# Kernel optimization log

Hardware: AMD Instinct MI355X
Metric: run time of the kernel (lower is better)

The kernel has to match this reference:

```python
import jax, jax.numpy as jnp
import numpy as np

B, T, C, H = 2, 2048, 1024, 16
HD = C // H  # head_dim = 64
NEG_INF = float('-inf')


def setup_inputs() -> dict:
    key = jax.random.key(0)
    ks = jax.random.split(key, 5)
    x = jax.random.normal(ks[0], (B, T, C), dtype=jnp.float32)
    # causal additive mask [T, T]: 0 on/below diagonal, -inf above
    causal = jnp.where(jnp.tril(jnp.ones((T, T), dtype=bool)), 0.0, NEG_INF).astype(jnp.float32)
    # pad the last 256 key positions of every batch element
    key_padding_mask = (jnp.arange(T)[None, :] >= (T - 256)) & jnp.ones((B, 1), dtype=bool)
    scale = 1.0 / np.sqrt(C)
    W_qkv = jax.random.normal(ks[1], (C, 3 * C), dtype=jnp.float32) * scale
    b_qkv = jnp.zeros((3 * C,), dtype=jnp.float32)
    W_out = jax.random.normal(ks[2], (C, C), dtype=jnp.float32) * scale
    b_out = jnp.zeros((C,), dtype=jnp.float32)
    return {
        'x': x,
        'attn_mask': causal,
        'key_padding_mask': key_padding_mask,
        'W_qkv': W_qkv,
        'b_qkv': b_qkv,
        'W_out': W_out,
        'b_out': b_out,
    }


def reference(x, attn_mask, key_padding_mask, W_qkv, b_qkv, W_out, b_out):
    Bx, Tx, Cx = x.shape
    # fused QKV projection -> [B, T, 3, H, HD]
    qkv = (x @ W_qkv + b_qkv).reshape(Bx, Tx, 3, H, HD)
    q = jnp.transpose(qkv[:, :, 0], (0, 2, 1, 3))  # [B, H, T, HD]
    k = jnp.transpose(qkv[:, :, 1], (0, 2, 1, 3))
    v = jnp.transpose(qkv[:, :, 2], (0, 2, 1, 3))
    # scores [B, H, T, T]
    scores = jnp.einsum('bhqd,bhkd->bhqk', q, k) / np.sqrt(HD)
    scores = scores + attn_mask[None, None, :, :]
    scores = jnp.where(key_padding_mask[:, None, None, :], NEG_INF, scores)
    probs = jax.nn.softmax(scores, axis=-1)
    out = jnp.einsum('bhqk,bhkd->bhqd', probs, v)  # [B, H, T, HD]
    out = jnp.transpose(out, (0, 2, 1, 3)).reshape(Bx, Tx, Cx)
    return out @ W_out + b_out
```

## Files before the change

kernel.cpp:

```cpp
#include <hip/hip_runtime.h>
#include <hip/hip_bf16.h>


typedef __attribute__((ext_vector_type(8))) short short8;
typedef __attribute__((ext_vector_type(4))) float f32x4;
typedef __attribute__((ext_vector_type(16))) float f32x16;
typedef __attribute__((ext_vector_type(4))) unsigned int u32x4;
typedef __attribute__((ext_vector_type(4))) unsigned short ushort4v;

#define MFMA_BF16 __builtin_amdgcn_mfma_f32_16x16x32_bf16
#define MFMA32 __builtin_amdgcn_mfma_f32_32x32x16_bf16
#define EXP2 __builtin_amdgcn_exp2f

__device__ __forceinline__ unsigned short f2bf(float f) {
  unsigned int u = __builtin_bit_cast(unsigned int, f);
  u += 0x7fffu + ((u >> 16) & 1u);
  return (unsigned short)(u >> 16);
}

__device__ __forceinline__ unsigned cvtpk_bf16(float lo, float hi) {
  unsigned r;
  asm("v_cvt_pk_bf16_f32 %0, %1, %2" : "=v"(r) : "v"(lo), "v"(hi));
  return r;
}

__device__ __forceinline__ short8 make_pa(unsigned cA, unsigned cB, unsigned cC, unsigned cD) {
  asm volatile("v_permlane32_swap_b32 %0, %1" : "+v"(cA), "+v"(cC));
  asm volatile("v_permlane32_swap_b32 %0, %1" : "+v"(cB), "+v"(cD));
  u32x4 wv = {cA, cB, cC, cD};
  return __builtin_bit_cast(short8, wv);
}

__device__ __forceinline__ void conv_x_body(const float* __restrict__ x,
                                            unsigned short* __restrict__ xb, int bid) {
  const int i = (bid * 256 + threadIdx.x) * 8;
  const float4 v0 = *reinterpret_cast<const float4*>(x + i);
  const float4 v1 = *reinterpret_cast<const float4*>(x + i + 4);
  short8 o;
  o[0] = (short)f2bf(v0.x); o[1] = (short)f2bf(v0.y);
  o[2] = (short)f2bf(v0.z); o[3] = (short)f2bf(v0.w);
  o[4] = (short)f2bf(v1.x); o[5] = (short)f2bf(v1.y);
  o[6] = (short)f2bf(v1.z); o[7] = (short)f2bf(v1.w);
  *reinterpret_cast<short8*>(xb + i) = o;
}

__device__ __forceinline__ void convT_body256(const float* __restrict__ W,
                                              unsigned short* __restrict__ WT,
                                              int Ncols, int bid, unsigned short* L) {
  const int t = threadIdx.x;
  const int kt = bid & 15, nt = bid >> 4;
  const int k0 = kt << 6, n0 = nt << 6;
#pragma unroll
  for (int it = 0; it < 4; ++it) {
    const int flat = it * 256 + t;
    const int kk = flat >> 4, c4 = (flat & 15) << 2;
    const float4 v = *reinterpret_cast<const float4*>(W + (k0 + kk) * Ncols + n0 + c4);
    L[(c4 + 0) * 72 + kk] = f2bf(v.x);
    L[(c4 + 1) * 72 + kk] = f2bf(v.y);
    L[(c4 + 2) * 72 + kk] = f2bf(v.z);
    L[(c4 + 3) * 72 + kk] = f2bf(v.w);
  }
  __syncthreads();
#pragma unroll
  for (int it = 0; it < 2; ++it) {
    const int flat = it * 256 + t;
    const int nn = flat >> 3, k8 = (flat & 7) << 3;
    *reinterpret_cast<short8*>(WT + (n0 + nn) * 1024 + k0 + k8) =
        *reinterpret_cast<const short8*>(&L[nn * 72 + k8]);
  }
}

__device__ __forceinline__ void convT_body512(const float* __restrict__ W,
                                              unsigned short* __restrict__ WT,
                                              int Ncols, int bid, unsigned short* L) {
  const int t = threadIdx.x;
  const int kt = bid & 15, nt = bid >> 4;
  const int k0 = kt << 6, n0 = nt << 6;
#pragma unroll
  for (int it = 0; it < 2; ++it) {
    const int flat = it * 512 + t;
    const int kk = flat >> 4, c4 = (flat & 15) << 2;
    const float4 v = *reinterpret_cast<const float4*>(W + (k0 + kk) * Ncols + n0 + c4);
    L[(c4 + 0) * 72 + kk] = f2bf(v.x);
    L[(c4 + 1) * 72 + kk] = f2bf(v.y);
    L[(c4 + 2) * 72 + kk] = f2bf(v.z);
    L[(c4 + 3) * 72 + kk] = f2bf(v.w);
  }
  __syncthreads();
  {
    const int nn = t >> 3, k8 = (t & 7) << 3;
    *reinterpret_cast<short8*>(WT + (n0 + nn) * 1024 + k0 + k8) =
        *reinterpret_cast<const short8*>(&L[nn * 72 + k8]);
  }
}

__global__ __launch_bounds__(256) void pre_kernel(const float* __restrict__ x,
                                                  unsigned short* __restrict__ xb,
                                                  const float* __restrict__ Wqkv,
                                                  unsigned short* __restrict__ WQT) {
  __shared__ unsigned short L[64 * 72];
  if (blockIdx.x < 2048) conv_x_body(x, xb, blockIdx.x);
  else convT_body256(Wqkv, WQT, 3072, blockIdx.x - 2048, L);
}

__device__ __forceinline__ void stage_tile512(const unsigned short* __restrict__ g,
                                              int row0, int k0,
                                              unsigned short* lds, int t) {
  const int lane = t & 63, w = t >> 6;
  const int rsub = lane >> 3;
  const int col16 = lane & 7;
#pragma unroll
  for (int i = 0; i < 2; ++i) {
    const int c = w * 2 + i;
    const int row = c * 8 + rsub;
    const unsigned short* gp =
        g + (row0 + row) * 1024 + k0 + ((col16 ^ rsub) << 3);
    unsigned short* lp = lds + c * 512;
    __builtin_amdgcn_global_load_lds(
        (const __attribute__((address_space(1))) unsigned int*)gp,
        (__attribute__((address_space(3))) unsigned int*)lp, 16, 0, 0);
  }
}

__device__ __forceinline__ short8 frag_read(const unsigned short* lds, int row, int colB) {
  return *reinterpret_cast<const short8*>(
      reinterpret_cast<const char*>(lds) + row * 128 + (colB ^ ((row & 7) << 4)));
}

__device__ __forceinline__ void gemm_step8(const unsigned short* Ab, const unsigned short* Bb,
                                           int wr, int wc, int lm, int lg, f32x4 acc[2][4]) {
#pragma unroll
  for (int ks = 0; ks < 2; ++ks) {
    short8 af[2], bfr[4];
#pragma unroll
    for (int i = 0; i < 2; ++i)
      af[i] = frag_read(Ab, wr * 32 + i * 16 + lm, ks * 64 + lg * 16);
#pragma unroll
    for (int j = 0; j < 4; ++j)
      bfr[j] = frag_read(Bb, wc * 64 + j * 16 + lm, ks * 64 + lg * 16);
#pragma unroll
    for (int i = 0; i < 2; ++i)
#pragma unroll
      for (int j = 0; j < 4; ++j)
        acc[i][j] = MFMA_BF16(af[i], bfr[j], acc[i][j], 0, 0, 0);
  }
}

__global__ __launch_bounds__(512, 4) void qkv_gemm_kernel(
    const unsigned short* __restrict__ xb,
    const unsigned short* __restrict__ Bt,
    const float* __restrict__ bias,
    unsigned short* __restrict__ ws) {
  __shared__ unsigned short LDSu[32768];
  const int t = threadIdx.x;
  const int bm = blockIdx.x & 31;
  const int bn = blockIdx.x >> 5;
  const int m0 = bm << 7, n0 = bn << 7;
  const int lane = t & 63, wid = t >> 6;
  const int wr = wid & 3, wc = wid >> 2;
  const int lm = lane & 15, lg = lane >> 4;
  f32x4 acc[2][4] = {};

  stage_tile512(xb, m0, 0, LDSu, t);
  stage_tile512(Bt, n0, 0, LDSu + 16384, t);
  asm volatile("s_waitcnt vmcnt(0)" ::: "memory");
  __syncthreads();
  for (int kt = 0; kt < 16; ++kt) {
    const int cur = kt & 1;
    if (kt < 15) {
      stage_tile512(xb, m0, (kt + 1) * 64, LDSu + (cur ^ 1) * 8192, t);
      stage_tile512(Bt, n0, (kt + 1) * 64, LDSu + 16384 + (cur ^ 1) * 8192, t);
    }
    gemm_step8(LDSu + cur * 8192, LDSu + 16384 + cur * 8192, wr, wc, lm, lg, acc);
    asm volatile("s_waitcnt vmcnt(0)" ::: "memory");
    __syncthreads();
  }

  const int which = n0 >> 10;
  if (which == 2) {
#pragma unroll
    for (int j = 0; j < 4; ++j) {
      const int col = wc * 64 + j * 16 + lm;
      const float bv = bias[n0 + col];
#pragma unroll
      for (int i = 0; i < 2; ++i)
#pragma unroll
        for (int r = 0; r < 4; ++r)
          LDSu[col * 136 + wr * 32 + i * 16 + lg * 4 + r] = f2bf(acc[i][j][r] + bv);
    }
    __syncthreads();
    const int bb = m0 >> 11, tt0 = m0 & 2047;
    unsigned short* dstbase = ws + 8388608 + bb * 2097152;
#pragma unroll
    for (int it = 0; it < 4; ++it) {
      const int flat = it * 512 + t;
      const int c = flat >> 4, r8 = (flat & 15) << 3;
      const short8 v = *reinterpret_cast<const short8*>(&LDSu[c * 136 + r8]);
      const int col0 = n0 + c;
      const int h = (col0 >> 6) & 15, d = col0 & 63;
      *reinterpret_cast<short8*>(dstbase + h * 131072 + d * 2048 + tt0 + r8) = v;
    }
  } else {
    const float scl = (which == 0) ? 0.18033688011112042f : 1.0f;
#pragma unroll
    for (int j = 0; j < 4; ++j) {
      const int col = wc * 64 + j * 16 + lm;
      const float bv = bias[n0 + col];
#pragma unroll
      for (int i = 0; i < 2; ++i)
#pragma unroll
        for (int r = 0; r < 4; ++r)
          LDSu[(wr * 32 + i * 16 + lg * 4 + r) * 136 + col] = f2bf((acc[i][j][r] + bv) * scl);
    }
    __syncthreads();
    unsigned short* dstbase = ws + which * 4194304;
#pragma unroll
    for (int it = 0; it < 4; ++it) {
      const int flat = it * 512 + t;
      const int row = flat >> 4, c = flat & 15;
      const short8 v = *reinterpret_cast<const short8*>(&LDSu[row * 136 + c * 8]);
      const int col0 = n0 + c * 8;
      const int h = (col0 >> 6) & 15, d = col0 & 63;
      const int grow = m0 + row;
      const int bb = grow >> 11, tt = grow & 2047;
      *reinterpret_cast<short8*>(dstbase + bb * 2097152 + h * 131072 + tt * 64 + d) = v;
    }
  }
}

__device__ __forceinline__ void stage_one(const unsigned short* __restrict__ src,
                                          int stride, unsigned short* lds, int t) {
  const int lane = t & 63;
  const int row = t >> 3;
  const int rsub = lane >> 3;
  const int col16 = lane & 7;
  const unsigned short* gp = src + row * stride + ((col16 ^ rsub) << 3);
  unsigned short* lp = lds + (t >> 6) * 512;
  __builtin_amdgcn_global_load_lds(
      (const __attribute__((address_space(1))) unsigned int*)gp,
      (__attribute__((address_space(3))) unsigned int*)lp, 16, 0, 0);
}

__device__ __forceinline__ short8 lds_frag64(const unsigned short* lds, int row, int colB) {
  return *reinterpret_cast<const short8*>(
      reinterpret_cast<const char*>(lds) + row * 128 + (colB ^ ((row & 7) << 4)));
}

__device__ __forceinline__ void attn_body(const unsigned short* __restrict__ qkv,
                                          unsigned short* __restrict__ att,
                                          unsigned short* S,
                                          int bid) {
  const int bh = bid & 31;
  const int grp = bid >> 5;
  const int qblk = (bid < 256) ? (15 - grp) : (grp - 8);
  const int q0blk = qblk << 7;
  const int t = threadIdx.x;
  const int w = t >> 6, w4 = w & 3, od = w >> 2;
  const int lane = t & 63;
  const int l31 = lane & 31, hi = lane >> 5;
  const int qrow_local = ((l31 >> 3) << 5) + (w4 << 3) + (l31 & 7);
  const int q_lane = q0blk + qrow_local;

  const unsigned short* Qp = qkv + bh * 131072;
  const unsigned short* Kp = qkv + 4194304 + bh * 131072;
  const unsigned short* Vtp = qkv + 8388608 + bh * 131072;
  unsigned short* KT = S;
  unsigned short* VT = S + 16384;

  short8 qf[4];
#pragma unroll
  for (int ds = 0; ds < 4; ++ds)
    qf[ds] = *reinterpret_cast<const short8*>(Qp + q_lane * 64 + ds * 16 + hi * 8);

  f32x16 o0, o1;
#pragma unroll
  for (int r = 0; r < 16; ++r) { o0[r] = 0.f; o1[r] = 0.f; }
  float mrun = -1e30f, lrun = 0.f;
  const int nkt_raw = 2 * qblk + 2;
  const int nkt = nkt_raw < 28 ? nkt_raw : 28;
  const int npair = nkt >> 1;
  const int qwmax = q0blk + 96 + (w4 << 3) + 7;
  const int qwmin = q0blk + (w4 << 3);

  stage_one(Kp, 64, KT, t);
  stage_one(Kp + 4096, 64, KT + 4096, t);
  stage_one(Vtp, 2048, VT, t);
  stage_one(Vtp + 64, 2048, VT + 4096, t);
  asm volatile("s_waitcnt vmcnt(0)" ::: "memory");
  __syncthreads();

  for (int i = 0; i < npair; ++i) {
    if (i + 1 < npair) {
      const int nb = (i + 1) & 1;
      stage_one(Kp + (2 * i + 2) * 4096, 64, KT + nb * 8192, t);
      stage_one(Kp + (2 * i + 3) * 4096, 64, KT + nb * 8192 + 4096, t);
      stage_one(Vtp + (2 * i + 2) * 64, 2048, VT + nb * 8192, t);
      stage_one(Vtp + (2 * i + 3) * 64, 2048, VT + nb * 8192 + 4096, t);
    }
    const int kt = 2 * i + od;
    const int k0 = kt << 6;
    if (k0 <= qwmax) {
      const unsigned short* Kl = KT + (i & 1) * 8192 + od * 4096;
      const unsigned short* Vl = VT + (i & 1) * 8192 + od * 4096;
      f32x16 s0, s1;
#pragma unroll
      for (int r = 0; r < 16; ++r) { s0[r] = 0.f; s1[r] = 0.f; }
      __builtin_amdgcn_s_setprio(1);
#pragma unroll
      for (int ds = 0; ds < 4; ++ds) {
        short8 ka = lds_frag64(Kl, l31, ds * 32 + hi * 16);
        short8 kb = lds_frag64(Kl, 32 + l31, ds * 32 + hi * 16);
        s0 = MFMA32(ka, qf[ds], s0, 0, 0, 0);
        s1 = MFMA32(kb, qf[ds], s1, 0, 0, 0);
      }
      __builtin_amdgcn_s_setprio(0);
      if (k0 + 63 > qwmin) {
        const int qrel = q_lane - k0;
        const int kb4 = hi << 2;
#pragma unroll
        for (int r = 0; r < 16; ++r) {
          const int cr = (r & 3) + ((r >> 2) << 3) + kb4;
          s0[r] = (cr > qrel) ? -1e30f : s0[r];
          s1[r] = (cr + 32 > qrel) ? -1e30f : s1[r];
        }
      }
      float mx[8];
#pragma unroll
      for (int r = 0; r < 8; ++r)
        mx[r] = fmaxf(fmaxf(s0[r], s0[r + 8]), fmaxf(s1[r], s1[r + 8]));
#pragma unroll
      for (int r = 0; r < 4; ++r) mx[r] = fmaxf(mx[r], mx[r + 4]);
      float mt = fmaxf(fmaxf(mx[0], mx[1]), fmaxf(mx[2], mx[3]));
      mt = fmaxf(mt, __shfl_xor(mt, 32));
      if (__any(mt > mrun + 8.f)) {
        const float mnew = fmaxf(mrun, mt);
        const float sf = EXP2(mrun - mnew);
        mrun = mnew;
        lrun *= sf;
#pragma unroll
        for (int r = 0; r < 16; ++r) { o0[r] *= sf; o1[r] *= sf; }
      }
#pragma unroll
      for (int r = 0; r < 16; ++r) {
        s0[r] = EXP2(s0[r] - mrun);
        s1[r] = EXP2(s1[r] - mrun);
      }
      float sm[8];
#pragma unroll
      for (int r = 0; r < 8; ++r)
        sm[r] = (s0[r] + s0[r + 8]) + (s1[r] + s1[r + 8]);
#pragma unroll
      for (int r = 0; r < 4; ++r) sm[r] += sm[r + 4];
      float rs = (sm[0] + sm[1]) + (sm[2] + sm[3]);
      rs += __shfl_xor(rs, 32);
      lrun += rs;
      unsigned c0[8], c1[8];
#pragma unroll
      for (int j = 0; j < 8; ++j) {
        c0[j] = cvtpk_bf16(s0[2 * j], s0[2 * j + 1]);
        c1[j] = cvtpk_bf16(s1[2 * j], s1[2 * j + 1]);
      }
      const short8 pa0 = make_pa(c0[0], c0[1], c0[2], c0[3]);
      const short8 pa1 = make_pa(c0[4], c0[5], c0[6], c0[7]);
      const short8 pa2 = make_pa(c1[0], c1[1], c1[2], c1[3]);
      const short8 pa3 = make_pa(c1[4], c1[5], c1[6], c1[7]);
      __builtin_amdgcn_s_setprio(1);
      {
        short8 va = lds_frag64(Vl, l31, 0 + hi * 16);
        short8 vb = lds_frag64(Vl, 32 + l31, 0 + hi * 16);
        o0 = MFMA32(va, pa0, o0, 0, 0, 0);
        o1 = MFMA32(vb, pa0, o1, 0, 0, 0);
      }
      {
        short8 va = lds_frag64(Vl, l31, 32 + hi * 16);
        short8 vb = lds_frag64(Vl, 32 + l31, 32 + hi * 16);
        o0 = MFMA32(va, pa1, o0, 0, 0, 0);
        o1 = MFMA32(vb, pa1, o1, 0, 0, 0);
      }
      {
        short8 va = lds_frag64(Vl, l31, 64 + hi * 16);
        short8 vb = lds_frag64(Vl, 32 + l31, 64 + hi * 16);
        o0 = MFMA32(va, pa2, o0, 0, 0, 0);
        o1 = MFMA32(vb, pa2, o1, 0, 0, 0);
      }
      {
        short8 va = lds_frag64(Vl, l31, 96 + hi * 16);
        short8 vb = lds_frag64(Vl, 32 + l31, 96 + hi * 16);
        o0 = MFMA32(va, pa3, o0, 0, 0, 0);
        o1 = MFMA32(vb, pa3, o1, 0, 0, 0);
      }
      __builtin_amdgcn_s_setprio(0);
    }
    asm volatile("s_waitcnt vmcnt(0)" ::: "memory");
    __syncthreads();
  }

  float* M = reinterpret_cast<float*>(S);
  if (od == 1) {
    float* Mb = M + (w4 * 64 + lane) * 36;
#pragma unroll
    for (int i2 = 0; i2 < 4; ++i2) {
      f32x4 a = {o0[4 * i2], o0[4 * i2 + 1], o0[4 * i2 + 2], o0[4 * i2 + 3]};
      f32x4 b = {o1[4 * i2], o1[4 * i2 + 1], o1[4 * i2 + 2], o1[4 * i2 + 3]};
      *reinterpret_cast<f32x4*>(Mb + 4 * i2) = a;
      *reinterpret_cast<f32x4*>(Mb + 16 + 4 * i2) = b;
    }
    Mb[32] = mrun;
    Mb[33] = lrun;
  }
  __syncthreads();
  if (od == 0) {
    const float* Mb = M + (w4 * 64 + lane) * 36;
    const float m_o = Mb[32], l_o = Mb[33];
    const float mstar = fmaxf(mrun, m_o);
    const float a = EXP2(mrun - mstar);
    const float bsc = EXP2(m_o - mstar);
    const float inv = 1.f / (lrun * a + l_o * bsc);
    const float fa = a * inv, fb = bsc * inv;
    const int bb = bh >> 4, h = bh & 15;
    unsigned short* ob = att + (bb * 2048 + q_lane) * 1024 + h * 64;
#pragma unroll
    for (int i = 0; i < 4; ++i) {
      ushort4v p0, p1;
#pragma unroll
      for (int r = 0; r < 4; ++r) {
        p0[r] = f2bf(o0[4 * i + r] * fa + Mb[4 * i + r] * fb);
        p1[r] = f2bf(o1[4 * i + r] * fa + Mb[16 + 4 * i + r] * fb);
      }
      const int d0 = 8 * i + 4 * hi;
      *reinterpret_cast<ushort4v*>(ob + d0) = p0;
      *reinterpret_cast<ushort4v*>(ob + 32 + d0) = p1;
    }
  }
}

__global__ __launch_bounds__(512, 4) void attn_wout_kernel(
    const unsigned short* __restrict__ qkv,
    unsigned short* __restrict__ att,
    const float* __restrict__ Wout,
    unsigned short* __restrict__ WOT) {
  __shared__ unsigned short S[32768];
  if (blockIdx.x < 512) attn_body(qkv, att, S, blockIdx.x);
  else convT_body512(Wout, WOT, 1024, blockIdx.x - 512, S);
}

__global__ __launch_bounds__(512, 4) void out_gemm_kernel(
    const unsigned short* __restrict__ A,
    const unsigned short* __restrict__ Bt,
    const float* __restrict__ bias,
    float* __restrict__ out) {
  __shared__ unsigned short LDSu[32768];
  const int t = threadIdx.x;
  const int bm = blockIdx.x & 31;
  const int bn = blockIdx.x >> 5;
  const int m0 = bm << 7, n0 = bn << 7;
  const int lane = t & 63, wid = t >> 6;
  const int wr = wid & 3, wc = wid >> 2;
  const int lm = lane & 15, lg = lane >> 4;
  f32x4 acc[2][4] = {};

  stage_tile512(A, m0, 0, LDSu, t);
  stage_tile512(Bt, n0, 0, LDSu + 16384, t);
  asm volatile("s_waitcnt vmcnt(0)" ::: "memory");
  __syncthreads();
  for (int kt = 0; kt < 16; ++kt) {
    const int cur = kt & 1;
    if (kt < 15) {
      stage_tile512(A, m0, (kt + 1) * 64, LDSu + (cur ^ 1) * 8192, t);
      stage_tile512(Bt, n0, (kt + 1) * 64, LDSu + 16384 + (cur ^ 1) * 8192, t);
    }
    gemm_step8(LDSu + cur * 8192, LDSu + 16384 + cur * 8192, wr, wc, lm, lg, acc);
    asm volatile("s_waitcnt vmcnt(0)" ::: "memory");
    __syncthreads();
  }

#pragma unroll
  for (int j = 0; j < 4; ++j) {
    const int col = n0 + wc * 64 + j * 16 + lm;
    const float bv = bias[col];
#pragma unroll
    for (int i = 0; i < 2; ++i) {
#pragma unroll
      for (int r = 0; r < 4; ++r) {
        const int row = m0 + wr * 32 + i * 16 + lg * 4 + r;
        out[row * 1024 + col] = acc[i][j][r] + bv;
      }
    }
  }
}

extern "C" void kernel_launch(void* const* d_in, const int* in_sizes, int n_in,
                              void* d_out, int out_size, void* d_ws, size_t ws_size,
                              hipStream_t stream) {
  const float* x    = (const float*)d_in[0];
  const float* Wqkv = (const float*)d_in[3];
  const float* bqkv = (const float*)d_in[4];
  const float* Wout = (const float*)d_in[5];
  const float* bout = (const float*)d_in[6];
  unsigned short* ws = (unsigned short*)d_ws;
  float* out = (float*)d_out;

  unsigned short* Qkv = ws;
  unsigned short* XB  = ws + 12582912;
  unsigned short* ATT = ws + 12582912;
  unsigned short* WQT = ws + 16777216;
  unsigned short* WOT = ws + 16777216;

  pre_kernel<<<dim3(2048 + 768), 256, 0, stream>>>(x, XB, Wqkv, WQT);
  qkv_gemm_kernel<<<dim3(768), 512, 0, stream>>>(XB, WQT, bqkv, Qkv);
  attn_wout_kernel<<<dim3(768), 512, 0, stream>>>(Qkv, ATT, Wout, WOT);
  out_gemm_kernel<<<dim3(256), 512, 0, stream>>>(ATT, WOT, bout, out);
}
```

Measured before the change: 84.32 us.

## Enlarge QKV GEMM tiles to 256x256 with interleaved staging and MFMA priority

The QKV projection GEMM moves from 128x128 to 256x256 output tiles per block. Each wave now holds 8x4 accumulators, which raises data reuse per LDS fragment and cuts the grid from 768 to 192 blocks. The next k-tile's global-to-LDS staging is split into four pieces that are interleaved with the MFMA groups, each preceded by a barrier, and s_setprio is raised around the MFMAs. The epilogue writes out in two 128-row halves through a reused LDS buffer. The cost is higher register and LDS use, so fewer waves can run per CU, and only 192 blocks may leave part of the 256 CUs idle.

```diff
diff --git a/kernel.cpp b/kernel.cpp
--- a/kernel.cpp
+++ b/kernel.cpp
@@ -146,32 +146,69 @@
   }
 }
 
-__global__ __launch_bounds__(512, 4) void qkv_gemm_kernel(
+__global__ __launch_bounds__(512, 2) void qkv_gemm_kernel(
     const unsigned short* __restrict__ xb,
     const unsigned short* __restrict__ Bt,
     const float* __restrict__ bias,
     unsigned short* __restrict__ ws) {
-  __shared__ unsigned short LDSu[32768];
+  __shared__ unsigned short LDSu[65536];
   const int t = threadIdx.x;
-  const int bm = blockIdx.x & 31;
-  const int bn = blockIdx.x >> 5;
-  const int m0 = bm << 7, n0 = bn << 7;
+  const int bm = blockIdx.x & 15;
+  const int bn = blockIdx.x >> 4;
+  const int m0 = bm << 8, n0 = bn << 8;
   const int lane = t & 63, wid = t >> 6;
-  const int wr = wid & 3, wc = wid >> 2;
+  const int wr = wid >> 2, wc = wid & 3;
   const int lm = lane & 15, lg = lane >> 4;
-  f32x4 acc[2][4] = {};
-
-  stage_tile512(xb, m0, 0, LDSu, t);
-  stage_tile512(Bt, n0, 0, LDSu + 16384, t);
+  f32x4 acc[8][4] = {};
+
+  unsigned short* LA = LDSu;
+  unsigned short* LB = LDSu + 32768;
+
+  stage_tile512(xb, m0,       0, LA, t);
+  stage_tile512(xb, m0 + 128, 0, LA + 8192, t);
+  stage_tile512(Bt, n0,       0, LB, t);
+  stage_tile512(Bt, n0 + 128, 0, LB + 8192, t);
   asm volatile("s_waitcnt vmcnt(0)" ::: "memory");
   __syncthreads();
+
+#pragma unroll 2
   for (int kt = 0; kt < 16; ++kt) {
-    const int cur = kt & 1;
-    if (kt < 15) {
-      stage_tile512(xb, m0, (kt + 1) * 64, LDSu + (cur ^ 1) * 8192, t);
-      stage_tile512(Bt, n0, (kt + 1) * 64, LDSu + 16384 + (cur ^ 1) * 8192, t);
-    }
-    gemm_step8(LDSu + cur * 8192, LDSu + 16384 + cur * 8192, wr, wc, lm, lg, acc);
+    const int p = kt & 1, np = p ^ 1;
+    const unsigned short* Aw = LA + p * 16384 + wr * 8192;
+    const unsigned short* Bw = LB + p * 16384 + (wc >> 1) * 8192;
+    const int brow0 = (wc & 1) * 64;
+    const int k1 = (kt + 1) << 6;
+    short8 bf[4][2];
+#pragma unroll
+    for (int j = 0; j < 4; ++j)
+#pragma unroll
+      for (int ks = 0; ks < 2; ++ks)
+        bf[j][ks] = frag_read(Bw, brow0 + j * 16 + lm, ks * 64 + lg * 16);
+#pragma unroll
+    for (int q = 0; q < 4; ++q) {
+      short8 aq[2][2];
+#pragma unroll
+      for (int i2 = 0; i2 < 2; ++i2)
+#pragma unroll
+        for (int ks = 0; ks < 2; ++ks)
+          aq[i2][ks] = frag_read(Aw, (2 * q + i2) * 16 + lm, ks * 64 + lg * 16);
+      if (kt < 15) {
+        if      (q == 0) stage_tile512(Bt, n0,       k1, LB + np * 16384, t);
+        else if (q == 1) stage_tile512(Bt, n0 + 128, k1, LB + np * 16384 + 8192, t);
+        else if (q == 2) stage_tile512(xb, m0,       k1, LA + np * 16384, t);
+        else             stage_tile512(xb, m0 + 128, k1, LA + np * 16384 + 8192, t);
+      }
+      __builtin_amdgcn_s_barrier();
+      __builtin_amdgcn_s_setprio(1);
+#pragma unroll
+      for (int i2 = 0; i2 < 2; ++i2)
+#pragma unroll
+        for (int j = 0; j < 4; ++j)
+#pragma unroll
+          for (int ks = 0; ks < 2; ++ks)
+            acc[2 * q + i2][j] = MFMA_BF16(aq[i2][ks], bf[j][ks], acc[2 * q + i2][j], 0, 0, 0);
+      __builtin_amdgcn_s_setprio(0);
+    }
     asm volatile("s_waitcnt vmcnt(0)" ::: "memory");
     __syncthreads();
   }
@@ -179,51 +216,65 @@
   const int which = n0 >> 10;
   if (which == 2) {
 #pragma unroll
-    for (int j = 0; j < 4; ++j) {
-      const int col = wc * 64 + j * 16 + lm;
-      const float bv = bias[n0 + col];
-#pragma unroll
-      for (int i = 0; i < 2; ++i)
-#pragma unroll
-        for (int r = 0; r < 4; ++r)
-          LDSu[col * 136 + wr * 32 + i * 16 + lg * 4 + r] = f2bf(acc[i][j][r] + bv);
-    }
-    __syncthreads();
-    const int bb = m0 >> 11, tt0 = m0 & 2047;
-    unsigned short* dstbase = ws + 8388608 + bb * 2097152;
-#pragma unroll
-    for (int it = 0; it < 4; ++it) {
-      const int flat = it * 512 + t;
-      const int c = flat >> 4, r8 = (flat & 15) << 3;
-      const short8 v = *reinterpret_cast<const short8*>(&LDSu[c * 136 + r8]);
-      const int col0 = n0 + c;
-      const int h = (col0 >> 6) & 15, d = col0 & 63;
-      *reinterpret_cast<short8*>(dstbase + h * 131072 + d * 2048 + tt0 + r8) = v;
+    for (int rh = 0; rh < 2; ++rh) {
+      __syncthreads();
+      if (wr == rh) {
+#pragma unroll
+        for (int j = 0; j < 4; ++j) {
+          const int col = wc * 64 + j * 16 + lm;
+          const float bv = bias[n0 + col];
+#pragma unroll
+          for (int i = 0; i < 8; ++i)
+#pragma unroll
+            for (int r = 0; r < 4; ++r)
+              LDSu[col * 136 + i * 16 + lg * 4 + r] = f2bf(acc[i][j][r] + bv);
+        }
+      }
+      __syncthreads();
+      const int grow0 = m0 + rh * 128;
+      const int bb = grow0 >> 11, tt0 = grow0 & 2047;
+      unsigned short* dstbase = ws + 8388608 + bb * 2097152;
+#pragma unroll
+      for (int it = 0; it < 8; ++it) {
+        const int flat = it * 512 + t;
+        const int c = flat >> 4, r8 = (flat & 15) << 3;
+        const short8 v = *reinterpret_cast<const short8*>(&LDSu[c * 136 + r8]);
+        const int col0 = n0 + c;
+        const int h = (col0 >> 6) & 15, d = col0 & 63;
+        *reinterpret_cast<short8*>(dstbase + h * 131072 + d * 2048 + tt0 + r8) = v;
+      }
     }
   } else {
     const float scl = (which == 0) ? 0.18033688011112042f : 1.0f;
-#pragma unroll
-    for (int j = 0; j < 4; ++j) {
-      const int col = wc * 64 + j * 16 + lm;
-      const float bv = bias[n0 + col];
-#pragma unroll
-      for (int i = 0; i < 2; ++i)
-#pragma unroll
-        for (int r = 0; r < 4; ++r)
-          LDSu[(wr * 32 + i * 16 + lg * 4 + r) * 136 + col] = f2bf((acc[i][j][r] + bv) * scl);
-    }
-    __syncthreads();
-    unsigned short* dstbase = ws + which * 4194304;
-#pragma unroll
-    for (int it = 0; it < 4; ++it) {
-      const int flat = it * 512 + t;
-      const int row = flat >> 4, c = flat & 15;
-      const short8 v = *reinterpret_cast<const short8*>(&LDSu[row * 136 + c * 8]);
-      const int col0 = n0 + c * 8;
-      const int h = (col0 >> 6) & 15, d = col0 & 63;
-      const int grow = m0 + row;
-      const int bb = grow >> 11, tt = grow & 2047;
-      *reinterpret_cast<short8*>(dstbase + bb * 2097152 + h * 131072 + tt * 64 + d) = v;
+    unsigned short* dstQK = ws + which * 4194304;
+#pragma unroll
+    for (int rh = 0; rh < 2; ++rh) {
+      __syncthreads();
+      if (wr == rh) {
+#pragma unroll
+        for (int j = 0; j < 4; ++j) {
+          const int col = wc * 64 + j * 16 + lm;
+          const float bv = bias[n0 + col];
+#pragma unroll
+          for (int i = 0; i < 8; ++i)
+#pragma unroll
+            for (int r = 0; r < 4; ++r)
+              LDSu[(i * 16 + lg * 4 + r) * 264 + col] = f2bf((acc[i][j][r] + bv) * scl);
+        }
+      }
+      __syncthreads();
+#pragma unroll
+      for (int it = 0; it < 8; ++it) {
+        const int flat = it * 512 + t;
+        const int row = flat >> 5;
+        const int c8 = (flat & 31) << 3;
+        const short8 v = *reinterpret_cast<const short8*>(&LDSu[row * 264 + c8]);
+        const int col0 = n0 + c8;
+        const int h = (col0 >> 6) & 15, d = col0 & 63;
+        const int grow = m0 + rh * 128 + row;
+        const int bb = grow >> 11, tt = grow & 2047;
+        *reinterpret_cast<short8*>(dstQK + bb * 2097152 + h * 131072 + tt * 64 + d) = v;
+      }
     }
   }
 }
@@ -507,7 +558,7 @@
   unsigned short* WOT = ws + 16777216;
 
   pre_kernel<<<dim3(2048 + 768), 256, 0, stream>>>(x, XB, Wqkv, WQT);
-  qkv_gemm_kernel<<<dim3(768), 512, 0, stream>>>(XB, WQT, bqkv, Qkv);
+  qkv_gemm_kernel<<<dim3(192), 512, 0, stream>>>(XB, WQT, bqkv, Qkv);
   attn_wout_kernel<<<dim3(768), 512, 0, stream>>>(Qkv, ATT, Wout, WOT);
   out_gemm_kernel<<<dim3(256), 512, 0, stream>>>(ATT, WOT, bout, out);
 }
```

New measurement: 88.74 us. 1.05x slower.
